# Kernel optimization log

Hardware: AMD Instinct MI355X
Metric: run time of the kernel (lower is better)

The kernel has to match this reference:

```python
import jax, jax.numpy as jnp
import numpy as np

IN_DIM = 512
OUT_DIM = 512
NUM_HARMONICS = 32
BATCH = 4096


def setup_inputs() -> dict:
    key = jax.random.key(0)
    k1, k2 = jax.random.split(key)
    x = jax.random.normal(k1, (BATCH, IN_DIM), dtype=jnp.float32)
    std = 1.0 / np.sqrt(IN_DIM * NUM_HARMONICS)
    fourier_coeffs = jax.random.normal(
        k2, (IN_DIM, NUM_HARMONICS, 2, OUT_DIM), dtype=jnp.float32) * std
    bias = jnp.zeros((OUT_DIM,), dtype=jnp.float32)
    return {"x": x, "fourier_coeffs": fourier_coeffs, "bias": bias}


def reference(x, fourier_coeffs, bias):
    # k = [1, ..., num_harmonics]
    k = jnp.arange(1, fourier_coeffs.shape[1] + 1, dtype=x.dtype)
    kx = x[:, :, None] * k                      # [b, i, g]
    trig = jnp.stack([jnp.cos(kx), jnp.sin(kx)], axis=-1)  # [b, i, g, 2]
    out = jnp.einsum('bigf,igfo->bo', trig, fourier_coeffs)
    return out + bias
```

## Files before the change

kernel.cpp:

```cpp
#include <hip/hip_runtime.h>
#include <hip/hip_bf16.h>
#include <stdint.h>
#include <stddef.h>

#define BATCH   4096
#define INDIM   512
#define OUTDIM  512
#define NH      32
#define KKDIM   64
#define INV2PI  0.15915494309189535f

#define BM       128
#define BN       256
#define THREADS  512
#define KSPLIT   4
#define DIMS_PER_WG (INDIM / KSPLIT)
#define CHUNK_ELEMS (BN * KKDIM)

#define B_BYTES   32768
#define A_STRIDE  72
#define A_BYTES   (BM * A_STRIDE * 2)
#define OFF_A0    (2 * B_BYTES)
#define OFF_X     (OFF_A0 + 2 * A_BYTES)
#define SMEM_BYTES (OFF_X + 2 * 8 * 128 * 4)

typedef short  bhalf8  __attribute__((ext_vector_type(8)));
typedef float  vfloat4 __attribute__((ext_vector_type(4)));

__device__ __forceinline__ unsigned pack_bf16(float a, float b) {
    union { __hip_bfloat162 h2; unsigned u; } cv;
    cv.h2 = __float22bfloat162_rn(float2{a, b});
    return cv.u;
}

__device__ __forceinline__ void async_copy16(const void* gsrc, void* ldst) {
    __builtin_amdgcn_global_load_lds(
        (const __attribute__((address_space(1))) void*)(uintptr_t)gsrc,
        (__attribute__((address_space(3))) void*)(uint32_t)(uintptr_t)ldst,
        16, 0, 0);
}

__global__ __launch_bounds__(256) void fkan_prepass(const float* __restrict__ coeffs,
                                                    unsigned short* __restrict__ Bt) {
    const int t  = threadIdx.x;
    const int cb = blockIdx.x & 1;
    const int i  = blockIdx.x >> 1;
    const float* __restrict__ src = coeffs + (size_t)i * (KKDIM * OUTDIM) + cb * BN;
    unsigned short* __restrict__ chunk = Bt + (size_t)(cb * INDIM + i) * CHUNK_ELEMS;
#pragma unroll
    for (int s = 0; s < 8; ++s) {
        const int unit = t + s * 256;
        const int col  = unit >> 3;
        const int pc   = unit & 7;
        const int kb   = (pc ^ (col & 7)) * 8;
        const float* p0 = src + (size_t)kb * OUTDIM + col;
        uint4 o;
        o.x = pack_bf16(p0[0 * OUTDIM], p0[1 * OUTDIM]);
        o.y = pack_bf16(p0[2 * OUTDIM], p0[3 * OUTDIM]);
        o.z = pack_bf16(p0[4 * OUTDIM], p0[5 * OUTDIM]);
        o.w = pack_bf16(p0[6 * OUTDIM], p0[7 * OUTDIM]);
        ((uint4*)chunk)[unit] = o;
    }
}

__global__ __launch_bounds__(256) void fkan_bias_init(const float* __restrict__ bias,
                                                      float* __restrict__ out) {
    const int idx = blockIdx.x * 256 + threadIdx.x;
    ((float4*)out)[idx] = ((const float4*)bias)[idx & 127];
}

__device__ __forceinline__ void stage_B(const unsigned short* __restrict__ Bt, char* smem,
                                        int cb, int dim_global, int parity, int t) {
    const char* chunk = (const char*)(Bt + (size_t)(cb * INDIM + dim_global) * CHUNK_ELEMS);
    char* bdst = smem + parity * B_BYTES;
#pragma unroll
    for (int s = 0; s < 4; ++s) {
        const int unit = t + s * 512;
        async_copy16(chunk + unit * 16, bdst + unit * 16);
    }
}

__device__ __forceinline__ void stage_x(const float* __restrict__ x, char* smem,
                                        int rowbase, int dimbase, int cn, int t) {
    const int r  = t >> 2;
    const int d0 = (t & 3) * 2;
    const float2 xv = *(const float2*)(x + (size_t)(rowbase + r) * INDIM + dimbase + cn * 8 + d0);
    float* xr = (float*)(smem + OFF_X + (cn & 1) * 4096);
    xr[(d0 + 0) * 128 + r] = xv.x * INV2PI;
    xr[(d0 + 1) * 128 + r] = xv.y * INV2PI;
}

__device__ __forceinline__ void do_trig(char* smem, int dim_local, int parity, int trow, int tq) {
    const float rv = ((const float*)(smem + OFF_X + ((dim_local >> 3) & 1) * 4096))
                     [(dim_local & 7) * 128 + trow];
    const float cd = __builtin_amdgcn_cosf(rv);
    const float sd = __builtin_amdgcn_sinf(rv);
    const float a0 = (float)(tq * 8 + 1) * rv;
    float c = __builtin_amdgcn_cosf(a0);
    float s = __builtin_amdgcn_sinf(a0);
    unsigned pk[8];
    pk[0] = pack_bf16(c, s);
#pragma unroll
    for (int j = 1; j < 8; ++j) {
        const float nc = c * cd - s * sd;
        const float ns = s * cd + c * sd;
        c = nc; s = ns;
        pk[j] = pack_bf16(c, s);
    }
    uint4* adst = (uint4*)(smem + OFF_A0 + parity * A_BYTES + trow * (A_STRIDE * 2) + tq * 32);
    uint4 w0; w0.x = pk[0]; w0.y = pk[1]; w0.z = pk[2]; w0.w = pk[3];
    uint4 w1; w1.x = pk[4]; w1.y = pk[5]; w1.z = pk[6]; w1.w = pk[7];
    adst[0] = w0;
    adst[1] = w1;
}

__global__ __launch_bounds__(THREADS, 2) void fkan_main(const float* __restrict__ x,
                                                        const unsigned short* __restrict__ Bt,
                                                        float* __restrict__ out) {
    __shared__ char smem[SMEM_BYTES];
    const int t      = threadIdx.x;
    const int grp    = blockIdx.x & 7;
    const int member = blockIdx.x >> 3;
    const int cb      = grp & 1;
    const int kq      = grp >> 1;
    const int rowbase = member * BM;
    const int colbase = cb * BN;
    const int dimbase = kq * DIMS_PER_WG;

    const int lane = t & 63;
    const int w    = t >> 6;
    const int wr   = w >> 2;
    const int wc   = w & 3;
    const int fr   = lane & 15;
    const int fq   = lane >> 4;
    const int fx   = lane & 7;

    const int trow = t & 127;
    const int tq   = t >> 7;

    vfloat4 acc[4][4];
#pragma unroll
    for (int a = 0; a < 4; ++a)
#pragma unroll
        for (int b = 0; b < 4; ++b) acc[a][b] = (vfloat4)0.0f;

    stage_x(x, smem, rowbase, dimbase, 0, t);
    __syncthreads();
    stage_B(Bt, smem, cb, dimbase + 0, 0, t);
    do_trig(smem, 0, 0, trow, tq);
    __syncthreads();

#pragma unroll 2
    for (int it = 0; it < DIMS_PER_WG; ++it) {
        const int p    = it & 1;
        const int inxt = it + 1;
        if (inxt < DIMS_PER_WG) {
            stage_B(Bt, smem, cb, dimbase + inxt, inxt & 1, t);
            if ((it & 7) == 0) {
                const int cn = (it >> 3) + 1;
                if (cn < 16) stage_x(x, smem, rowbase, dimbase, cn, t);
            }
            do_trig(smem, inxt, inxt & 1, trow, tq);
        }
        {
            const char* Ab = smem + OFF_A0 + p * A_BYTES;
            const char* Bb = smem + p * B_BYTES;
#pragma unroll
            for (int ks = 0; ks < 2; ++ks) {
                bhalf8 av[4], bv[4];
#pragma unroll
                for (int rt = 0; rt < 4; ++rt)
                    av[rt] = *(const bhalf8*)(Ab + (wr * 64 + rt * 16 + fr) * (A_STRIDE * 2)
                                                 + ks * 64 + fq * 16);
#pragma unroll
                for (int ct = 0; ct < 4; ++ct)
                    bv[ct] = *(const bhalf8*)(Bb + (wc * 64 + ct * 16 + fr) * 128
                                                 + (((ks * 4 + fq) ^ fx) * 16));
#pragma unroll
                for (int rt = 0; rt < 4; ++rt)
#pragma unroll
                    for (int ct = 0; ct < 4; ++ct)
                        acc[rt][ct] = __builtin_amdgcn_mfma_f32_16x16x32_bf16(
                            av[rt], bv[ct], acc[rt][ct], 0, 0, 0);
            }
        }
        __syncthreads();
    }

#pragma unroll
    for (int rt = 0; rt < 4; ++rt) {
#pragma unroll
        for (int ct = 0; ct < 4; ++ct) {
            const int col  = colbase + wc * 64 + ct * 16 + fr;
            const int row0 = rowbase + wr * 64 + rt * 16 + fq * 4;
#pragma unroll
            for (int r = 0; r < 4; ++r)
                atomicAdd(out + (size_t)(row0 + r) * OUTDIM + col, acc[rt][ct][r]);
        }
    }
}

__global__ __launch_bounds__(256) void fkan_naive(const float* __restrict__ x,
                                                  const float* __restrict__ coeffs,
                                                  const float* __restrict__ bias,
                                                  float* __restrict__ out) {
    const int b = blockIdx.x >> 1;
    const int o = ((blockIdx.x & 1) << 8) + threadIdx.x;
    float acc = bias[o];
    const float* xrow = x + (size_t)b * INDIM;
    for (int i = 0; i < INDIM; ++i) {
        const float rv = xrow[i] * INV2PI;
        const float cd = __builtin_amdgcn_cosf(rv);
        const float sd = __builtin_amdgcn_sinf(rv);
        float c = cd, s = sd;
        const float* cp = coeffs + (size_t)i * (KKDIM * OUTDIM) + o;
#pragma unroll 4
        for (int g = 0; g < NH; ++g) {
            acc += c * cp[g * 2 * OUTDIM] + s * cp[(g * 2 + 1) * OUTDIM];
            const float nc = c * cd - s * sd;
            const float ns = s * cd + c * sd;
            c = nc; s = ns;
        }
    }
    out[(size_t)b * OUTDIM + o] = acc;
}

extern "C" void kernel_launch(void* const* d_in, const int* in_sizes, int n_in,
                              void* d_out, int out_size, void* d_ws, size_t ws_size,
                              hipStream_t stream) {
    (void)in_sizes; (void)n_in; (void)out_size;
    const float* x      = (const float*)d_in[0];
    const float* coeffs = (const float*)d_in[1];
    const float* bias   = (const float*)d_in[2];
    float* out          = (float*)d_out;

    const size_t bt_bytes = (size_t)2 * INDIM * CHUNK_ELEMS * sizeof(unsigned short);
    if (ws_size >= bt_bytes) {
        unsigned short* Bt = (unsigned short*)d_ws;
        fkan_prepass<<<2 * INDIM, 256, 0, stream>>>(coeffs, Bt);
        fkan_bias_init<<<(BATCH * OUTDIM) / (4 * 256), 256, 0, stream>>>(bias, out);
        fkan_main<<<(BATCH / BM) * 2 * KSPLIT, THREADS, 0, stream>>>(x, Bt, out);
    } else {
        fkan_naive<<<BATCH * 2, 256, 0, stream>>>(x, coeffs, bias, out);
    }
}
```

Baseline: 295.1 us.

## Double row tile to 256, raise K-split to 8, swizzle A tile, stage prepass via LDS

The main kernel's row tile grows from 128 to 256, so each staged B chunk is reused by twice as many rows. The K split rises from 4 to 8 to keep the grid size unchanged. The A tile moves from a padded layout to an XOR-swizzled 128-byte row layout, and each thread now computes 16 harmonics instead of 8. The prepass now reads the coefficients coalesced into LDS before transposing. The cost is twice the accumulator registers (8x4 tiles) and more atomic adds to the output, which may hurt occupancy at 2 blocks per CU.

```diff
diff --git a/kernel.cpp b/kernel.cpp
--- a/kernel.cpp
+++ b/kernel.cpp
@@ -10,19 +10,19 @@
 #define KKDIM   64
 #define INV2PI  0.15915494309189535f
 
-#define BM       128
+#define BM       256
 #define BN       256
 #define THREADS  512
-#define KSPLIT   4
+#define KSPLIT   8
 #define DIMS_PER_WG (INDIM / KSPLIT)
 #define CHUNK_ELEMS (BN * KKDIM)
 
 #define B_BYTES   32768
-#define A_STRIDE  72
-#define A_BYTES   (BM * A_STRIDE * 2)
+#define A_BYTES   (BM * 128)
 #define OFF_A0    (2 * B_BYTES)
 #define OFF_X     (OFF_A0 + 2 * A_BYTES)
-#define SMEM_BYTES (OFF_X + 2 * 8 * 128 * 4)
+#define X_CHUNK_BYTES (8 * BM * 4)
+#define SMEM_BYTES (OFF_X + 2 * X_CHUNK_BYTES)
 
 typedef short  bhalf8  __attribute__((ext_vector_type(8)));
 typedef float  vfloat4 __attribute__((ext_vector_type(4)));
@@ -42,23 +42,31 @@
 
 __global__ __launch_bounds__(256) void fkan_prepass(const float* __restrict__ coeffs,
                                                     unsigned short* __restrict__ Bt) {
+    __shared__ float lds[64][260];
     const int t  = threadIdx.x;
     const int cb = blockIdx.x & 1;
     const int i  = blockIdx.x >> 1;
     const float* __restrict__ src = coeffs + (size_t)i * (KKDIM * OUTDIM) + cb * BN;
     unsigned short* __restrict__ chunk = Bt + (size_t)(cb * INDIM + i) * CHUNK_ELEMS;
 #pragma unroll
+    for (int rd = 0; rd < 16; ++rd) {
+        const int r  = rd * 4 + (t >> 6);
+        const int c4 = (t & 63) * 4;
+        const float4 v = *(const float4*)(src + (size_t)r * OUTDIM + c4);
+        *(float4*)&lds[r][c4] = v;
+    }
+    __syncthreads();
+#pragma unroll
     for (int s = 0; s < 8; ++s) {
         const int unit = t + s * 256;
         const int col  = unit >> 3;
         const int pc   = unit & 7;
         const int kb   = (pc ^ (col & 7)) * 8;
-        const float* p0 = src + (size_t)kb * OUTDIM + col;
         uint4 o;
-        o.x = pack_bf16(p0[0 * OUTDIM], p0[1 * OUTDIM]);
-        o.y = pack_bf16(p0[2 * OUTDIM], p0[3 * OUTDIM]);
-        o.z = pack_bf16(p0[4 * OUTDIM], p0[5 * OUTDIM]);
-        o.w = pack_bf16(p0[6 * OUTDIM], p0[7 * OUTDIM]);
+        o.x = pack_bf16(lds[kb + 0][col], lds[kb + 1][col]);
+        o.y = pack_bf16(lds[kb + 2][col], lds[kb + 3][col]);
+        o.z = pack_bf16(lds[kb + 4][col], lds[kb + 5][col]);
+        o.w = pack_bf16(lds[kb + 6][col], lds[kb + 7][col]);
         ((uint4*)chunk)[unit] = o;
     }
 }
@@ -82,36 +90,43 @@
 
 __device__ __forceinline__ void stage_x(const float* __restrict__ x, char* smem,
                                         int rowbase, int dimbase, int cn, int t) {
-    const int r  = t >> 2;
-    const int d0 = (t & 3) * 2;
-    const float2 xv = *(const float2*)(x + (size_t)(rowbase + r) * INDIM + dimbase + cn * 8 + d0);
-    float* xr = (float*)(smem + OFF_X + (cn & 1) * 4096);
-    xr[(d0 + 0) * 128 + r] = xv.x * INV2PI;
-    xr[(d0 + 1) * 128 + r] = xv.y * INV2PI;
+    const int r  = t >> 1;
+    const int d0 = (t & 1) * 4;
+    const float4 xv = *(const float4*)(x + (size_t)(rowbase + r) * INDIM + dimbase + cn * 8 + d0);
+    float* xr = (float*)(smem + OFF_X + (cn & 1) * X_CHUNK_BYTES);
+    xr[(d0 + 0) * BM + r] = xv.x * INV2PI;
+    xr[(d0 + 1) * BM + r] = xv.y * INV2PI;
+    xr[(d0 + 2) * BM + r] = xv.z * INV2PI;
+    xr[(d0 + 3) * BM + r] = xv.w * INV2PI;
 }
 
 __device__ __forceinline__ void do_trig(char* smem, int dim_local, int parity, int trow, int tq) {
-    const float rv = ((const float*)(smem + OFF_X + ((dim_local >> 3) & 1) * 4096))
-                     [(dim_local & 7) * 128 + trow];
+    const float rv = ((const float*)(smem + OFF_X + ((dim_local >> 3) & 1) * X_CHUNK_BYTES))
+                     [(dim_local & 7) * BM + trow];
     const float cd = __builtin_amdgcn_cosf(rv);
     const float sd = __builtin_amdgcn_sinf(rv);
-    const float a0 = (float)(tq * 8 + 1) * rv;
+    const float a0 = (float)(tq * 16 + 1) * rv;
     float c = __builtin_amdgcn_cosf(a0);
     float s = __builtin_amdgcn_sinf(a0);
-    unsigned pk[8];
+    unsigned pk[16];
     pk[0] = pack_bf16(c, s);
 #pragma unroll
-    for (int j = 1; j < 8; ++j) {
+    for (int j = 1; j < 16; ++j) {
         const float nc = c * cd - s * sd;
         const float ns = s * cd + c * sd;
         c = nc; s = ns;
         pk[j] = pack_bf16(c, s);
     }
-    uint4* adst = (uint4*)(smem + OFF_A0 + parity * A_BYTES + trow * (A_STRIDE * 2) + tq * 32);
-    uint4 w0; w0.x = pk[0]; w0.y = pk[1]; w0.z = pk[2]; w0.w = pk[3];
-    uint4 w1; w1.x = pk[4]; w1.y = pk[5]; w1.z = pk[6]; w1.w = pk[7];
-    adst[0] = w0;
-    adst[1] = w1;
+    uint4* abase = (uint4*)(smem + OFF_A0 + parity * A_BYTES + trow * 128);
+    const int sw = trow & 7;
+    uint4 w0; w0.x = pk[0];  w0.y = pk[1];  w0.z = pk[2];  w0.w = pk[3];
+    uint4 w1; w1.x = pk[4];  w1.y = pk[5];  w1.z = pk[6];  w1.w = pk[7];
+    uint4 w2; w2.x = pk[8];  w2.y = pk[9];  w2.z = pk[10]; w2.w = pk[11];
+    uint4 w3; w3.x = pk[12]; w3.y = pk[13]; w3.z = pk[14]; w3.w = pk[15];
+    abase[(tq * 4 + 0) ^ sw] = w0;
+    abase[(tq * 4 + 1) ^ sw] = w1;
+    abase[(tq * 4 + 2) ^ sw] = w2;
+    abase[(tq * 4 + 3) ^ sw] = w3;
 }
 
 __global__ __launch_bounds__(THREADS, 2) void fkan_main(const float* __restrict__ x,
@@ -119,8 +134,8 @@
                                                         float* __restrict__ out) {
     __shared__ char smem[SMEM_BYTES];
     const int t      = threadIdx.x;
-    const int grp    = blockIdx.x & 7;
-    const int member = blockIdx.x >> 3;
+    const int grp    = blockIdx.x & 15;
+    const int member = blockIdx.x >> 4;
     const int cb      = grp & 1;
     const int kq      = grp >> 1;
     const int rowbase = member * BM;
@@ -135,12 +150,12 @@
     const int fq   = lane >> 4;
     const int fx   = lane & 7;
 
-    const int trow = t & 127;
-    const int tq   = t >> 7;
-
-    vfloat4 acc[4][4];
-#pragma unroll
-    for (int a = 0; a < 4; ++a)
+    const int trow = t >> 1;
+    const int tq   = t & 1;
+
+    vfloat4 acc[8][4];
+#pragma unroll
+    for (int a = 0; a < 8; ++a)
 #pragma unroll
         for (int b = 0; b < 4; ++b) acc[a][b] = (vfloat4)0.0f;
 
@@ -158,7 +173,7 @@
             stage_B(Bt, smem, cb, dimbase + inxt, inxt & 1, t);
             if ((it & 7) == 0) {
                 const int cn = (it >> 3) + 1;
-                if (cn < 16) stage_x(x, smem, rowbase, dimbase, cn, t);
+                if (cn < 8) stage_x(x, smem, rowbase, dimbase, cn, t);
             }
             do_trig(smem, inxt, inxt & 1, trow, tq);
         }
@@ -167,32 +182,31 @@
             const char* Bb = smem + p * B_BYTES;
 #pragma unroll
             for (int ks = 0; ks < 2; ++ks) {
-                bhalf8 av[4], bv[4];
-#pragma unroll
-                for (int rt = 0; rt < 4; ++rt)
-                    av[rt] = *(const bhalf8*)(Ab + (wr * 64 + rt * 16 + fr) * (A_STRIDE * 2)
-                                                 + ks * 64 + fq * 16);
+                bhalf8 bv[4];
 #pragma unroll
                 for (int ct = 0; ct < 4; ++ct)
                     bv[ct] = *(const bhalf8*)(Bb + (wc * 64 + ct * 16 + fr) * 128
                                                  + (((ks * 4 + fq) ^ fx) * 16));
 #pragma unroll
-                for (int rt = 0; rt < 4; ++rt)
+                for (int rt = 0; rt < 8; ++rt) {
+                    const bhalf8 av = *(const bhalf8*)(Ab + (wr * 128 + rt * 16 + fr) * 128
+                                                          + (((ks * 4 + fq) ^ fx) * 16));
 #pragma unroll
                     for (int ct = 0; ct < 4; ++ct)
                         acc[rt][ct] = __builtin_amdgcn_mfma_f32_16x16x32_bf16(
-                            av[rt], bv[ct], acc[rt][ct], 0, 0, 0);
+                            av, bv[ct], acc[rt][ct], 0, 0, 0);
+                }
             }
         }
         __syncthreads();
     }
 
 #pragma unroll
-    for (int rt = 0; rt < 4; ++rt) {
+    for (int rt = 0; rt < 8; ++rt) {
 #pragma unroll
         for (int ct = 0; ct < 4; ++ct) {
             const int col  = colbase + wc * 64 + ct * 16 + fr;
-            const int row0 = rowbase + wr * 64 + rt * 16 + fq * 4;
+            const int row0 = rowbase + wr * 128 + rt * 16 + fq * 4;
 #pragma unroll
             for (int r = 0; r < 4; ++r)
                 atomicAdd(out + (size_t)(row0 + r) * OUTDIM + col, acc[rt][ct][r]);
```

Result: faster. 277.1 us (-6.1%).
